# Kernel optimization log

Measured on AMD Instinct MI355X. Metric: run time of the kernel, lower is better.

## Reference

```python
import jax, jax.numpy as jnp
import numpy as np

N_NODES = 100000
N_EDGES = 800000
D_IN = 16
D_OUT = 16


def setup_inputs() -> dict:
    key = jax.random.key(0)
    k1, k2, k3, k4, k5, k6 = jax.random.split(key, 6)
    x = jax.random.normal(k1, (N_NODES, D_IN), dtype=jnp.float32)
    edge_index = jax.random.randint(k2, (2, N_EDGES), 0, N_NODES, dtype=jnp.int64)
    # kaiming-uniform-like scale: bound = sqrt(3/fan_in) with a=1 -> sqrt(6/(2*fan_in))
    bound = float(np.sqrt(3.0 / D_IN))
    weight_edge = jax.random.uniform(k3, (N_EDGES, D_OUT, D_IN), jnp.float32, -bound, bound)
    weight_self = jax.random.uniform(k4, (N_NODES, D_OUT, D_IN), jnp.float32, -bound, bound)
    bias_edge = jnp.zeros((N_EDGES, D_OUT), dtype=jnp.float32)
    bias_self = jnp.zeros((N_NODES, D_OUT), dtype=jnp.float32)
    return {
        "x": x,
        "edge_index": edge_index,
        "weight_edge": weight_edge,
        "weight_self": weight_self,
        "bias_edge": bias_edge,
        "bias_self": bias_self,
    }


def reference(x, edge_index, weight_edge, weight_self, bias_edge, bias_self):
    # Self-loop term: per-node matvec x_i' = W_self_i @ x_i + b_self_i
    out = jnp.einsum("ni,noi->no", x, weight_self) + bias_self
    # Edge messages: gather src features, per-edge matvec, scatter-add to dst
    src, dst = edge_index[0], edge_index[1]
    edge_contrib = jnp.einsum("ei,eoi->eo", x[src], weight_edge) + bias_edge
    out = out + jax.ops.segment_sum(edge_contrib, dst, num_segments=x.shape[0])
    return jax.nn.relu(out)
```

## Files before the change

### kernel.cpp

```cpp
#include <hip/hip_runtime.h>


#define DD 16

__global__ void sheaf_self_kernel(const float* __restrict__ x,
                                  const float* __restrict__ w_self,
                                  const float* __restrict__ b_self,
                                  float* __restrict__ out,
                                  int n_nodes) {
    const int lane  = threadIdx.x & 63;
    const int wave  = (int)((blockIdx.x * blockDim.x + threadIdx.x) >> 6);
    const int nwav  = (int)((gridDim.x * blockDim.x) >> 6);
    const int qi    = lane & 3;

    for (int n = wave; n < n_nodes; n += nwav) {
        const float4 w  = *(const float4*)(w_self + (size_t)n * (DD * DD) + lane * 4);
        const float4 xv = *(const float4*)(x      + (size_t)n * DD + qi * 4);
        float p = w.x * xv.x + w.y * xv.y + w.z * xv.z + w.w * xv.w;
        p += __shfl_xor(p, 1);
        p += __shfl_xor(p, 2);
        float v = __shfl(p, (lane & 15) * 4);
        if (lane < DD) {
            out[(size_t)n * DD + lane] = v + b_self[(size_t)n * DD + lane];
        }
    }
}

__global__ void sheaf_edge_kernel(const float* __restrict__ x,
                                  const int* __restrict__ edge_index,
                                  const float* __restrict__ w_edge,
                                  const float* __restrict__ b_edge,
                                  float* __restrict__ out,
                                  int n_edges) {
    const int lane  = threadIdx.x & 63;
    const int wave  = (int)((blockIdx.x * blockDim.x + threadIdx.x) >> 6);
    const int nwav  = (int)((gridDim.x * blockDim.x) >> 6);
    const int qi    = lane & 3;

    for (int e = wave; e < n_edges; e += nwav) {
        const int src = edge_index[e];
        const int dst = edge_index[n_edges + e];
        const float4 w  = *(const float4*)(w_edge + (size_t)e * (DD * DD) + lane * 4);
        const float4 xv = *(const float4*)(x + (size_t)src * DD + qi * 4);
        float p = w.x * xv.x + w.y * xv.y + w.z * xv.z + w.w * xv.w;
        p += __shfl_xor(p, 1);
        p += __shfl_xor(p, 2);
        float v = __shfl(p, (lane & 15) * 4);
        if (lane < DD) {
            atomicAdd(&out[(size_t)dst * DD + lane],
                      v + b_edge[(size_t)e * DD + lane]);
        }
    }
}

__global__ void sheaf_relu_kernel(float* __restrict__ out, int total4) {
    int i = (int)(blockIdx.x * blockDim.x + threadIdx.x);
    const int stride = (int)(gridDim.x * blockDim.x);
    for (; i < total4; i += stride) {
        float4 v = ((float4*)out)[i];
        v.x = fmaxf(v.x, 0.f);
        v.y = fmaxf(v.y, 0.f);
        v.z = fmaxf(v.z, 0.f);
        v.w = fmaxf(v.w, 0.f);
        ((float4*)out)[i] = v;
    }
}

extern "C" void kernel_launch(void* const* d_in, const int* in_sizes, int n_in,
                              void* d_out, int out_size, void* d_ws, size_t ws_size,
                              hipStream_t stream) {
    const float* x       = (const float*)d_in[0];
    const int*   ei      = (const int*)  d_in[1];
    const float* w_edge  = (const float*)d_in[2];
    const float* w_self  = (const float*)d_in[3];
    const float* b_edge  = (const float*)d_in[4];
    const float* b_self  = (const float*)d_in[5];
    float*       out     = (float*)d_out;

    const int n_nodes = in_sizes[0] / DD;
    const int n_edges = in_sizes[1] / 2;

    sheaf_self_kernel<<<1024, 256, 0, stream>>>(x, w_self, b_self, out, n_nodes);
    sheaf_edge_kernel<<<2048, 256, 0, stream>>>(x, ei, w_edge, b_edge, out, n_edges);
    sheaf_relu_kernel<<<512, 256, 0, stream>>>(out, n_nodes * DD / 4);
}
```

Measured before the change: 1.151 ms.

## Map one thread per output row instead of one wave per edge/node

Each edge (and node) is now handled by 16 threads, each loading a full 16-float weight row plus the source feature vector and computing its dot product directly, which removes the wave-level shuffle reduction and the 48 of 64 lanes that sat idle at the store/atomic. The grid-stride loops become one-thread-per-output launches sized to the problem. In exchange, each thread issues strided 64-byte row loads and the x row is read redundantly by 16 threads, which depends on cache hits.

After: 1.124 ms. 1.02x faster.

```diff
diff --git a/kernel.cpp b/kernel.cpp
--- a/kernel.cpp
+++ b/kernel.cpp
@@ -8,22 +8,23 @@
                                   const float* __restrict__ b_self,
                                   float* __restrict__ out,
                                   int n_nodes) {
-    const int lane  = threadIdx.x & 63;
-    const int wave  = (int)((blockIdx.x * blockDim.x + threadIdx.x) >> 6);
-    const int nwav  = (int)((gridDim.x * blockDim.x) >> 6);
-    const int qi    = lane & 3;
+    const int t = (int)(blockIdx.x * blockDim.x + threadIdx.x);
+    const int n = t >> 4;
+    const int o = t & 15;
+    if (n >= n_nodes) return;
 
-    for (int n = wave; n < n_nodes; n += nwav) {
-        const float4 w  = *(const float4*)(w_self + (size_t)n * (DD * DD) + lane * 4);
-        const float4 xv = *(const float4*)(x      + (size_t)n * DD + qi * 4);
-        float p = w.x * xv.x + w.y * xv.y + w.z * xv.z + w.w * xv.w;
-        p += __shfl_xor(p, 1);
-        p += __shfl_xor(p, 2);
-        float v = __shfl(p, (lane & 15) * 4);
-        if (lane < DD) {
-            out[(size_t)n * DD + lane] = v + b_self[(size_t)n * DD + lane];
-        }
-    }
+    const float4* wr = (const float4*)(w_self + (size_t)n * (DD * DD) + o * DD);
+    const float4* xr = (const float4*)(x + (size_t)n * DD);
+    float4 w0 = wr[0], w1 = wr[1], w2 = wr[2], w3 = wr[3];
+    float4 x0 = xr[0], x1 = xr[1], x2 = xr[2], x3 = xr[3];
+
+    float acc = b_self[(size_t)n * DD + o];
+    acc += w0.x * x0.x + w0.y * x0.y + w0.z * x0.z + w0.w * x0.w;
+    acc += w1.x * x1.x + w1.y * x1.y + w1.z * x1.z + w1.w * x1.w;
+    acc += w2.x * x2.x + w2.y * x2.y + w2.z * x2.z + w2.w * x2.w;
+    acc += w3.x * x3.x + w3.y * x3.y + w3.z * x3.z + w3.w * x3.w;
+
+    out[(size_t)n * DD + o] = acc;
 }
 
 __global__ void sheaf_edge_kernel(const float* __restrict__ x,
@@ -32,55 +33,65 @@
                                   const float* __restrict__ b_edge,
                                   float* __restrict__ out,
                                   int n_edges) {
-    const int lane  = threadIdx.x & 63;
-    const int wave  = (int)((blockIdx.x * blockDim.x + threadIdx.x) >> 6);
-    const int nwav  = (int)((gridDim.x * blockDim.x) >> 6);
-    const int qi    = lane & 3;
+    const int t = (int)(blockIdx.x * blockDim.x + threadIdx.x);
+    const int e = t >> 4;
+    const int o = t & 15;
+    if (e >= n_edges) return;
 
-    for (int e = wave; e < n_edges; e += nwav) {
-        const int src = edge_index[e];
-        const int dst = edge_index[n_edges + e];
-        const float4 w  = *(const float4*)(w_edge + (size_t)e * (DD * DD) + lane * 4);
-        const float4 xv = *(const float4*)(x + (size_t)src * DD + qi * 4);
-        float p = w.x * xv.x + w.y * xv.y + w.z * xv.z + w.w * xv.w;
-        p += __shfl_xor(p, 1);
-        p += __shfl_xor(p, 2);
-        float v = __shfl(p, (lane & 15) * 4);
-        if (lane < DD) {
-            atomicAdd(&out[(size_t)dst * DD + lane],
-                      v + b_edge[(size_t)e * DD + lane]);
-        }
-    }
+    const int src = edge_index[e];
+    const int dst = edge_index[n_edges + e];
+
+    const float4* wr = (const float4*)(w_edge + (size_t)e * (DD * DD) + o * DD);
+    const float4* xr = (const float4*)(x + (size_t)src * DD);
+    float4 w0 = wr[0], w1 = wr[1], w2 = wr[2], w3 = wr[3];
+    float4 x0 = xr[0], x1 = xr[1], x2 = xr[2], x3 = xr[3];
+
+    float acc = b_edge[(size_t)e * DD + o];
+    acc += w0.x * x0.x + w0.y * x0.y + w0.z * x0.z + w0.w * x0.w;
+    acc += w1.x * x1.x + w1.y * x1.y + w1.z * x1.z + w1.w * x1.w;
+    acc += w2.x * x2.x + w2.y * x2.y + w2.z * x2.z + w2.w * x2.w;
+    acc += w3.x * x3.x + w3.y * x3.y + w3.z * x3.z + w3.w * x3.w;
+
+    atomicAdd(&out[(size_t)dst * DD + o], acc);
 }
 
 __global__ void sheaf_relu_kernel(float* __restrict__ out, int total4) {
-    int i = (int)(blockIdx.x * blockDim.x + threadIdx.x);
-    const int stride = (int)(gridDim.x * blockDim.x);
-    for (; i < total4; i += stride) {
-        float4 v = ((float4*)out)[i];
-        v.x = fmaxf(v.x, 0.f);
-        v.y = fmaxf(v.y, 0.f);
-        v.z = fmaxf(v.z, 0.f);
-        v.w = fmaxf(v.w, 0.f);
-        ((float4*)out)[i] = v;
-    }
+    const int i = (int)(blockIdx.x * blockDim.x + threadIdx.x);
+    if (i >= total4) return;
+    float4 v = ((float4*)out)[i];
+    v.x = fmaxf(v.x, 0.f);
+    v.y = fmaxf(v.y, 0.f);
+    v.z = fmaxf(v.z, 0.f);
+    v.w = fmaxf(v.w, 0.f);
+    ((float4*)out)[i] = v;
 }
 
 extern "C" void kernel_launch(void* const* d_in, const int* in_sizes, int n_in,
                               void* d_out, int out_size, void* d_ws, size_t ws_size,
                               hipStream_t stream) {
-    const float* x       = (const float*)d_in[0];
-    const int*   ei      = (const int*)  d_in[1];
-    const float* w_edge  = (const float*)d_in[2];
-    const float* w_self  = (const float*)d_in[3];
-    const float* b_edge  = (const float*)d_in[4];
-    const float* b_self  = (const float*)d_in[5];
-    float*       out     = (float*)d_out;
+    const float* x      = (const float*)d_in[0];
+    const int*   ei     = (const int*)  d_in[1];
+    const float* w_edge = (const float*)d_in[2];
+    const float* w_self = (const float*)d_in[3];
+    const float* b_edge = (const float*)d_in[4];
+    const float* b_self = (const float*)d_in[5];
+    float*       out    = (float*)d_out;
 
     const int n_nodes = in_sizes[0] / DD;
     const int n_edges = in_sizes[1] / 2;
 
-    sheaf_self_kernel<<<1024, 256, 0, stream>>>(x, w_self, b_self, out, n_nodes);
-    sheaf_edge_kernel<<<2048, 256, 0, stream>>>(x, ei, w_edge, b_edge, out, n_edges);
-    sheaf_relu_kernel<<<512, 256, 0, stream>>>(out, n_nodes * DD / 4);
+    {
+        const int threads = n_nodes * DD;
+        sheaf_self_kernel<<<(threads + 255) / 256, 256, 0, stream>>>(
+            x, w_self, b_self, out, n_nodes);
+    }
+    {
+        const int threads = n_edges * DD;
+        sheaf_edge_kernel<<<(threads + 255) / 256, 256, 0, stream>>>(
+            x, ei, w_edge, b_edge, out, n_edges);
+    }
+    {
+        const int total4 = n_nodes * DD / 4;
+        sheaf_relu_kernel<<<(total4 + 255) / 256, 256, 0, stream>>>(out, total4);
+    }
 }
```
